# Kernel optimization log

Hardware: AMD Instinct MI355X
Metric: run time of the kernel (lower is better)

## Reference

```python
import jax, jax.numpy as jnp
import numpy as np

B, S, D, H = 16, 577, 1280, 16
HD = D // H  # 80
HALF = HD // 2  # 40


def setup_inputs() -> dict:
    key = jax.random.key(0)
    ks = jax.random.split(key, 8)
    hidden_states = jax.random.normal(ks[0], (B, S, D), dtype=jnp.float32)
    # 2D rotary frequencies: random angles -> unit-magnitude complex rotations
    angles = jax.random.uniform(ks[1], (S, HALF), dtype=jnp.float32) * (2.0 * np.pi)
    freqs_cos = jnp.cos(angles)
    freqs_sin = jnp.sin(angles)
    scale = 1.0 / np.sqrt(D)
    Wq = jax.random.normal(ks[2], (D, D), dtype=jnp.float32) * scale
    Wk = jax.random.normal(ks[3], (D, D), dtype=jnp.float32) * scale
    Wv = jax.random.normal(ks[4], (D, D), dtype=jnp.float32) * scale
    Wo = jax.random.normal(ks[5], (D, D), dtype=jnp.float32) * scale
    z = jnp.zeros((D,), dtype=jnp.float32)
    return {
        "hidden_states": hidden_states,
        "freqs_cos": freqs_cos,
        "freqs_sin": freqs_sin,
        "Wq": Wq, "bq": z, "Wk": Wk, "bk": z,
        "Wv": Wv, "bv": z, "Wo": Wo, "bo": z,
    }


def _apply_rotary(x, cos, sin):
    # x: [B,S,H,HD]; cos/sin: [S, HD/2]; interleaved complex pairs (even=real, odd=imag)
    xr = x[..., 0::2]
    xi = x[..., 1::2]
    c = cos[None, :, None, :]
    s = sin[None, :, None, :]
    out_r = xr * c - xi * s
    out_i = xr * s + xi * c
    # re-interleave pairs back to [..., HD]
    return jnp.stack([out_r, out_i], axis=-1).reshape(x.shape)


def reference(hidden_states, freqs_cos, freqs_sin, Wq, bq, Wk, bk, Wv, bv, Wo, bo):
    q = (hidden_states @ Wq.T + bq).reshape(B, S, H, HD)
    k = (hidden_states @ Wk.T + bk).reshape(B, S, H, HD)
    v = (hidden_states @ Wv.T + bv).reshape(B, S, H, HD)
    q = _apply_rotary(q, freqs_cos, freqs_sin)
    k = _apply_rotary(k, freqs_cos, freqs_sin)
    # [B,H,S,HD]
    q = q.transpose(0, 2, 1, 3)
    k = k.transpose(0, 2, 1, 3)
    v = v.transpose(0, 2, 1, 3)
    scale = 1.0 / np.sqrt(HD).astype(np.float32)
    scores = jnp.einsum("bhsd,bhtd->bhst", q, k) * scale
    probs = jax.nn.softmax(scores, axis=-1)
    attn = jnp.einsum("bhst,bhtd->bhsd", probs, v)
    attn = attn.transpose(0, 2, 1, 3).reshape(B, S, D)
    return attn @ Wo.T + bo
```

## Files before the change

### kernel.cpp

```cpp
#include <hip/hip_runtime.h>

#define B_N 16
#define S_N 577
#define D_N 1280
#define H_N 16
#define HD_N 80
#define HALF_N 40
#define M_N 9232
#define M_PAD 9344
#define M_PAD2 9472
#define K_N 1280
#define VT_S 608
#define QSCALE 0.11180339887498949f

typedef __bf16 bf16_t;
typedef bf16_t bf16x8 __attribute__((ext_vector_type(8)));
typedef float f32x4 __attribute__((ext_vector_type(4)));

__device__ __forceinline__ float bf2f(unsigned short u) {
    union { unsigned int i; float f; } x; x.i = ((unsigned int)u) << 16; return x.f;
}
__device__ __forceinline__ unsigned short f2bf(float f) {
    union { unsigned int i; float f; } x; x.f = f;
    unsigned int r = x.i + 0x7FFFu + ((x.i >> 16) & 1u);
    return (unsigned short)(r >> 16);
}

__device__ __forceinline__ void gld_lds16(const unsigned short* g, unsigned short* l) {
    __builtin_amdgcn_global_load_lds(
        (const __attribute__((address_space(1))) unsigned int*)g,
        (__attribute__((address_space(3))) unsigned int*)l,
        16, 0, 0);
}

__global__ __launch_bounds__(256) void cvt_kernel(const float* __restrict__ in,
                                                  unsigned short* __restrict__ out, int n4) {
    int i = blockIdx.x * 256 + threadIdx.x;
    if (i < n4) {
        float4 v = ((const float4*)in)[i];
        ushort4 o;
        o.x = f2bf(v.x); o.y = f2bf(v.y); o.z = f2bf(v.z); o.w = f2bf(v.w);
        ((ushort4*)out)[i] = o;
    }
}

#define W4_N (D_N * K_N / 4)
__global__ __launch_bounds__(256) void cvt4_kernel(
    const float* __restrict__ w0, const float* __restrict__ w1,
    const float* __restrict__ w2, const float* __restrict__ w3,
    unsigned short* __restrict__ out) {
    int i = blockIdx.x * 256 + threadIdx.x;
    if (i >= 4 * W4_N) return;
    int r = i / W4_N, j = i - r * W4_N;
    const float* src = (r == 0) ? w0 : (r == 1) ? w1 : (r == 2) ? w2 : w3;
    float4 v = ((const float4*)src)[j];
    ushort4 o;
    o.x = f2bf(v.x); o.y = f2bf(v.y); o.z = f2bf(v.z); o.w = f2bf(v.w);
    ((ushort4*)out)[i] = o;
}

#define PHASE_MFMA(AFR, BFR, MB) do {                                          \
    __builtin_amdgcn_s_setprio(1);                                             \
    _Pragma("unroll")                                                          \
    for (int mf_ = 0; mf_ < 4; ++mf_) {                                        \
        _Pragma("unroll")                                                      \
        for (int nf_ = 0; nf_ < 4; ++nf_)                                      \
            acc[(MB) + mf_][nf_] = __builtin_amdgcn_mfma_f32_16x16x32_bf16(    \
                (AFR)[mf_], (BFR)[nf_], acc[(MB) + mf_][nf_], 0, 0, 0);        \
    }                                                                          \
    __builtin_amdgcn_s_setprio(0);                                             \
} while (0)

#define BARRIER() do {                                                         \
    asm volatile("" ::: "memory");                                             \
    __builtin_amdgcn_s_barrier();                                              \
    __builtin_amdgcn_sched_barrier(0);                                         \
    asm volatile("" ::: "memory");                                             \
} while (0)

#define VMCNT8() do { asm volatile("s_waitcnt vmcnt(8)" ::: "memory"); } while (0)

#define KHALF(S, KK, ST_ODD, ST_EVEN) do {                                     \
    bf16x8 bfr[4], af[4];                                                      \
    _Pragma("unroll")                                                          \
    for (int f_ = 0; f_ < 4; ++f_) bfr[f_] = rdB(S, KK, f_);                   \
    _Pragma("unroll")                                                          \
    for (int f_ = 0; f_ < 4; ++f_) af[f_] = rdA(S, KK, f_);                    \
    ST_ODD;                                                                    \
    PHASE_MFMA(af, bfr, 0);                                                    \
    BARRIER();                                                                 \
    _Pragma("unroll")                                                          \
    for (int f_ = 0; f_ < 4; ++f_) af[f_] = rdA(S, KK, 4 + f_);                \
    ST_EVEN;                                                                   \
    PHASE_MFMA(af, bfr, 4);                                                    \
    VMCNT8();                                                                  \
    BARRIER();                                                                 \
} while (0)

__global__ __launch_bounds__(512, 2) void mgemm256_kernel(
    const unsigned short* __restrict__ A,
    const unsigned short* __restrict__ Wb,
    const float* __restrict__ b0, const float* __restrict__ b1,
    const float* __restrict__ b2,
    const float* __restrict__ cosb, const float* __restrict__ sinb,
    void* __restrict__ o0, void* __restrict__ o1, void* __restrict__ o2)
{
    extern __shared__ unsigned short smem[];
    unsigned short* const Asb = smem;
    unsigned short* const Bsb = smem + 4 * 8192;

    const int tid = threadIdx.x;
    const int wave = tid >> 6, lane = tid & 63;
    const int quad = lane >> 4, n = lane & 15;
    const int wm = wave >> 2, wn = wave & 3;
    const int m0 = blockIdx.y * 256, n0g = blockIdx.x * 256;

    const int srow = wave * 16 + (lane >> 2);
    const int scb  = (lane & 3) ^ ((lane >> 2) & 3);

    const unsigned short* gA = A  + (size_t)(m0  + srow) * K_N + scb * 8;
    const unsigned short* gB = Wb + (size_t)(n0g + srow) * K_N + scb * 8;

    f32x4 acc[8][4] = {};

    auto stA = [&](int s, int h, int kt) {
        unsigned short* l = Asb + (s * 2 + h) * 8192 + wave * 512;
        const unsigned short* g = gA + kt * 64 + h * 32;
        gld_lds16(g, l);
        gld_lds16(g + (size_t)128 * K_N, l + 4096);
    };
    auto stB = [&](int s, int h, int kt) {
        unsigned short* l = Bsb + (s * 2 + h) * 8192 + wave * 512;
        const unsigned short* g = gB + kt * 64 + h * 32;
        gld_lds16(g, l);
        gld_lds16(g + (size_t)128 * K_N, l + 4096);
    };

    const int sa_blk = (quad ^ (n & 3)) * 8;
    auto rdA = [&](int s, int kk, int mf) {
        return *(const bf16x8*)&Asb[(s * 2 + kk) * 8192 +
                                    (wm * 128 + mf * 16 + n) * 32 + sa_blk];
    };
    auto rdB = [&](int s, int kk, int nf) {
        return *(const bf16x8*)&Bsb[(s * 2 + kk) * 8192 +
                                    (wn * 64 + nf * 16 + n) * 32 + sa_blk];
    };

    stA(0, 0, 0); stB(0, 0, 0); stA(0, 1, 0); stB(0, 1, 0); stA(1, 0, 1); stB(1, 0, 1);
    VMCNT8();
    BARRIER();

    #pragma unroll 1
    for (int i = 0; i < 10; ++i) {
        const int tb  = 2 * i + 1;
        const int ta2 = (2 * i + 2 > 19) ? 19 : 2 * i + 2;
        const int tb2 = (2 * i + 3 > 19) ? 19 : 2 * i + 3;
        KHALF(0, 0, stA(1, 1, tb),  stB(1, 1, tb));
        KHALF(0, 1, stA(0, 0, ta2), stB(0, 0, ta2));
        KHALF(1, 0, stA(0, 1, ta2), stB(0, 1, ta2));
        KHALF(1, 1, stA(1, 0, tb2), stB(1, 0, tb2));
    }
    asm volatile("s_waitcnt vmcnt(0)" ::: "memory");

    const int wsel = blockIdx.x / 5;
    const float* bias = (wsel == 0) ? b0 : (wsel == 1) ? b1 : b2;
    unsigned short* out =
        (unsigned short*)((wsel == 0) ? o0 : (wsel == 1) ? o1 : o2);
    const int nloc0 = n0g - wsel * 1280 + wn * 64;
    const bool evn = (n & 1) == 0;

    #pragma unroll
    for (int mf = 0; mf < 8; ++mf) {
        #pragma unroll
        for (int r = 0; r < 4; ++r) {
            const int mrow = m0 + wm * 128 + mf * 16 + quad * 4 + r;
            const int b = mrow / S_N, s = mrow - b * S_N;
            const bool ok = mrow < M_N;
            #pragma unroll
            for (int nf = 0; nf < 4; ++nf) {
                const int ncol = nloc0 + nf * 16 + n;
                const int h = ncol / HD_N, hd = ncol - h * HD_N;
                float v = acc[mf][nf][r] + bias[ncol];
                if (wsel == 2) {
                    if (ok)
                        out[((size_t)(b * H_N + h) * HD_N + hd) * VT_S + s] = f2bf(v);
                } else {
                    float pv = __shfl_xor(v, 1);
                    float c  = cosb[s * HALF_N + (hd >> 1)];
                    float sn = sinb[s * HALF_N + (hd >> 1)];
                    float res = evn ? (v * c - pv * sn) : (pv * sn + v * c);
                    if (wsel == 0) res *= QSCALE;
                    if (ok)
                        out[((size_t)(b * H_N + h) * S_N + s) * HD_N + hd] = f2bf(res);
                }
            }
        }
    }
}

template <int MODE>
__global__ __launch_bounds__(256) void mgemm64_kernel(
    const unsigned short* __restrict__ A,
    const unsigned short* __restrict__ Wb,
    const float* __restrict__ b0,
    const float* __restrict__ cosb, const float* __restrict__ sinb,
    void* __restrict__ o0)
{
    __shared__ __align__(16) unsigned short As[2][128 * 64];
    __shared__ __align__(16) unsigned short Bs[2][128 * 64];

    const int tid = threadIdx.x;
    const int wave = tid >> 6, lane = tid & 63;
    const int quad = lane >> 4, n = lane & 15;
    const int wm = wave >> 1, wn = wave & 1;
    const int m0 = blockIdx.y * 128, n0g = blockIdx.x * 128;

    const int srow = lane >> 3;
    const int scol = (((lane & 7) ^ srow) * 8);

    const unsigned short* gA = A + (size_t)(m0 + wave * 32 + srow) * K_N + scol;
    const unsigned short* gB = Wb + (size_t)(n0g + wave * 32 + srow) * K_N + scol;
    const int lofs = wave * 32 * 64;

    f32x4 acc[4][4] = {};

    auto stage = [&](int pp, int k0) {
        unsigned short* lA = &As[pp][lofs];
        unsigned short* lB = &Bs[pp][lofs];
        #pragma unroll
        for (int i = 0; i < 4; ++i) {
            gld_lds16(gA + k0 + i * 8 * K_N, lA + i * 512);
            gld_lds16(gB + k0 + i * 8 * K_N, lB + i * 512);
        }
    };

    auto compute = [&](int pp) {
        #pragma unroll
        for (int kk = 0; kk < 2; ++kk) {
            const int sa = ((((kk << 2) | quad) ^ (n & 7)) * 8);
            bf16x8 af[4], bfr[4];
            #pragma unroll
            for (int mt = 0; mt < 4; ++mt)
                af[mt] = *(const bf16x8*)&As[pp][(wm * 64 + mt * 16 + n) * 64 + sa];
            #pragma unroll
            for (int nt = 0; nt < 4; ++nt)
                bfr[nt] = *(const bf16x8*)&Bs[pp][(wn * 64 + nt * 16 + n) * 64 + sa];
            #pragma unroll
            for (int mt = 0; mt < 4; ++mt)
                #pragma unroll
                for (int nt = 0; nt < 4; ++nt)
                    acc[mt][nt] = __builtin_amdgcn_mfma_f32_16x16x32_bf16(
                        af[mt], bfr[nt], acc[mt][nt], 0, 0, 0);
        }
    };

    stage(0, 0);

    #pragma unroll 2
    for (int t = 0; t < 19; ++t) {
        const int pp = t & 1;
        stage(pp ^ 1, (t + 1) * 64);
        asm volatile("s_waitcnt vmcnt(8)" ::: "memory");
        __builtin_amdgcn_s_barrier();
        compute(pp);
        __builtin_amdgcn_s_barrier();
    }
    asm volatile("s_waitcnt vmcnt(0)" ::: "memory");
    __builtin_amdgcn_s_barrier();
    compute(1);

    const int mbase = m0 + wm * 64;
    const int nbase = n0g + wn * 64;
    float* outp = (float*)o0;
    #pragma unroll
    for (int mt = 0; mt < 4; ++mt)
        #pragma unroll
        for (int nt = 0; nt < 4; ++nt) {
            const int ncol = nbase + nt * 16 + n;
            const float bv = b0[ncol];
            #pragma unroll
            for (int r = 0; r < 4; ++r) {
                int mrow = mbase + mt * 16 + quad * 4 + r;
                if (mrow < M_N)
                    outp[(size_t)mrow * D_N + ncol] = acc[mt][nt][r] + bv;
            }
        }
}

__global__ __launch_bounds__(256) void fattn_kernel(
    const unsigned short* __restrict__ qb,
    const unsigned short* __restrict__ kb,
    const unsigned short* __restrict__ vt,
    unsigned short* __restrict__ attn)
{
    __shared__ __align__(16) unsigned short Plds[4][2][2][16 * 32];

    const int tid = threadIdx.x;
    const int wave = tid >> 6, lane = tid & 63;
    const int quad = lane >> 4, n = lane & 15;

    const int bid = blockIdx.x;
    const int xcd = bid & 7, t = bid >> 3;
    const int qt = t % 5, hl = t / 5;
    const int bh = hl * 8 + xcd;
    const int q0 = qt * 128 + wave * 32;

    const bf16x8 zf{};
    const unsigned short* qrow0 = qb + ((size_t)bh * S_N + q0 + n) * HD_N;
    const unsigned short* qrow1 = qrow0 + 16 * HD_N;
    bf16x8 aq00 = *(const bf16x8*)(qrow0 + quad * 8);
    bf16x8 aq01 = *(const bf16x8*)(qrow0 + 32 + quad * 8);
    bf16x8 aq02 = (quad < 2) ? *(const bf16x8*)(qrow0 + 64 + quad * 8) : zf;
    bf16x8 aq10 = *(const bf16x8*)(qrow1 + quad * 8);
    bf16x8 aq11 = *(const bf16x8*)(qrow1 + 32 + quad * 8);
    bf16x8 aq12 = (quad < 2) ? *(const bf16x8*)(qrow1 + 64 + quad * 8) : zf;

    const bf16_t one = (bf16_t)1.0f;
    const bf16x8 vones_all = {one, one, one, one, one, one, one, one};
    const bf16x8 vones = (n == 0) ? vones_all : zf;

    f32x4 o0[6] = {};
    f32x4 o1[6] = {};

    const unsigned short* kbase = kb + (size_t)bh * S_N * HD_N;
    const unsigned short* vbase = vt + (size_t)bh * HD_N * VT_S;

    #pragma unroll 2
    for (int t0 = 0; t0 < 608; t0 += 32) {
        const int pp = (t0 >> 5) & 1;
        unsigned short* pl0 = &Plds[wave][pp][0][0];
        unsigned short* pl1 = &Plds[wave][pp][1][0];

        const unsigned short* krA = kbase + (size_t)(t0 + n) * HD_N;
        const unsigned short* krB = krA + 16 * HD_N;
        bf16x8 bA0 = *(const bf16x8*)(krA + quad * 8);
        bf16x8 bA1 = *(const bf16x8*)(krA + 32 + quad * 8);
        bf16x8 bA2 = (quad < 2) ? *(const bf16x8*)(krA + 64 + quad * 8) : zf;
        bf16x8 bB0 = *(const bf16x8*)(krB + quad * 8);
        bf16x8 bB1 = *(const bf16x8*)(krB + 32 + quad * 8);
        bf16x8 bB2 = (quad < 2) ? *(const bf16x8*)(krB + 64 + quad * 8) : zf;

        f32x4 c00{}, c01{}, c10{}, c11{};
        c00 = __builtin_amdgcn_mfma_f32_16x16x32_bf16(aq00, bA0, c00, 0, 0, 0);
        c00 = __builtin_amdgcn_mfma_f32_16x16x32_bf16(aq01, bA1, c00, 0, 0, 0);
        c00 = __builtin_amdgcn_mfma_f32_16x16x32_bf16(aq02, bA2, c00, 0, 0, 0);
        c01 = __builtin_amdgcn_mfma_f32_16x16x32_bf16(aq00, bB0, c01, 0, 0, 0);
        c01 = __builtin_amdgcn_mfma_f32_16x16x32_bf16(aq01, bB1, c01, 0, 0, 0);
        c01 = __builtin_amdgcn_mfma_f32_16x16x32_bf16(aq02, bB2, c01, 0, 0, 0);
        c10 = __builtin_amdgcn_mfma_f32_16x16x32_bf16(aq10, bA0, c10, 0, 0, 0);
        c10 = __builtin_amdgcn_mfma_f32_16x16x32_bf16(aq11, bA1, c10, 0, 0, 0);
        c10 = __builtin_amdgcn_mfma_f32_16x16x32_bf16(aq12, bA2, c10, 0, 0, 0);
        c11 = __builtin_amdgcn_mfma_f32_16x16x32_bf16(aq10, bB0, c11, 0, 0, 0);
        c11 = __builtin_amdgcn_mfma_f32_16x16x32_bf16(aq11, bB1, c11, 0, 0, 0);
        c11 = __builtin_amdgcn_mfma_f32_16x16x32_bf16(aq12, bB2, c11, 0, 0, 0);

        const bool mA = (t0 + n) >= S_N;
        const bool mB = (t0 + 16 + n) >= S_N;

        #pragma unroll
        for (int r = 0; r < 4; ++r) {
            float p00 = mA ? 0.0f : __expf(c00[r]);
            float p01 = mB ? 0.0f : __expf(c01[r]);
            float p10 = mA ? 0.0f : __expf(c10[r]);
            float p11 = mB ? 0.0f : __expf(c11[r]);
            pl0[(quad * 4 + r) * 32 + n]      = f2bf(p00);
            pl0[(quad * 4 + r) * 32 + 16 + n] = f2bf(p01);
            pl1[(quad * 4 + r) * 32 + n]      = f2bf(p10);
            pl1[(quad * 4 + r) * 32 + 16 + n] = f2bf(p11);
        }

        bf16x8 ap0 = *(const bf16x8*)(pl0 + n * 32 + quad * 8);
        bf16x8 ap1 = *(const bf16x8*)(pl1 + n * 32 + quad * 8);

        #pragma unroll
        for (int nt = 0; nt < 5; ++nt) {
            const unsigned short* vr = vbase + (size_t)(nt * 16 + n) * VT_S + t0 + quad * 8;
            bf16x8 bv = *(const bf16x8*)vr;
            o0[nt] = __builtin_amdgcn_mfma_f32_16x16x32_bf16(ap0, bv, o0[nt], 0, 0, 0);
            o1[nt] = __builtin_amdgcn_mfma_f32_16x16x32_bf16(ap1, bv, o1[nt], 0, 0, 0);
        }
        o0[5] = __builtin_amdgcn_mfma_f32_16x16x32_bf16(ap0, vones, o0[5], 0, 0, 0);
        o1[5] = __builtin_amdgcn_mfma_f32_16x16x32_bf16(ap1, vones, o1[5], 0, 0, 0);
    }

    const int b = bh >> 4, h = bh & 15;
    #pragma unroll
    for (int r = 0; r < 4; ++r) {
        float l0 = __shfl(o0[5][r], lane & 48);
        float l1 = __shfl(o1[5][r], lane & 48);
        float linv0 = 1.0f / l0, linv1 = 1.0f / l1;
        int s0 = q0 + quad * 4 + r;
        int s1 = s0 + 16;
        #pragma unroll
        for (int nt = 0; nt < 5; ++nt) {
            if (s0 < S_N)
                attn[((size_t)b * S_N + s0) * D_N + h * HD_N + nt * 16 + n] =
                    f2bf(o0[nt][r] * linv0);
            if (s1 < S_N)
                attn[((size_t)b * S_N + s1) * D_N + h * HD_N + nt * 16 + n] =
                    f2bf(o1[nt][r] * linv1);
        }
    }
}

extern "C" void kernel_launch(void* const* d_in, const int* in_sizes, int n_in,
                              void* d_out, int out_size, void* d_ws, size_t ws_size,
                              hipStream_t stream) {
    const float* hs = (const float*)d_in[0];
    const float* fc = (const float*)d_in[1];
    const float* fs = (const float*)d_in[2];
    const float* Wq = (const float*)d_in[3];
    const float* bq = (const float*)d_in[4];
    const float* Wk = (const float*)d_in[5];
    const float* bk = (const float*)d_in[6];
    const float* Wv = (const float*)d_in[7];
    const float* bv = (const float*)d_in[8];
    const float* Wo = (const float*)d_in[9];
    const float* bo = (const float*)d_in[10];
    float* out = (float*)d_out;

    char* ws = (char*)d_ws;
    size_t off = 0;
    auto alloc = [&](size_t bytes) {
        char* p = ws + off; off += (bytes + 255) & ~(size_t)255; return p;
    };
    unsigned short* hsb  = (unsigned short*)alloc((size_t)M_PAD2 * K_N * 2);
    unsigned short* qb   = (unsigned short*)alloc((size_t)M_N * K_N * 2 + 32768);
    unsigned short* kb   = (unsigned short*)alloc((size_t)M_N * K_N * 2 + 32768);
    unsigned short* vt   = (unsigned short*)alloc((size_t)B_N * H_N * HD_N * VT_S * 2);
    unsigned short* Wall = (unsigned short*)alloc((size_t)4 * D_N * K_N * 2);

    const int HS4 = M_N * K_N / 4;
    dim3 blk(256);

    cvt_kernel<<<(HS4 + 255) / 256, blk, 0, stream>>>(hs, hsb, HS4);
    cvt4_kernel<<<(4 * W4_N + 255) / 256, blk, 0, stream>>>(Wq, Wk, Wv, Wo, Wall);

    (void)hipFuncSetAttribute(reinterpret_cast<const void*>(&mgemm256_kernel),
                              hipFuncAttributeMaxDynamicSharedMemorySize, 131072);
    mgemm256_kernel<<<dim3(15, 37), dim3(512), 131072, stream>>>(
        hsb, Wall, bq, bk, bv, fc, fs, qb, kb, vt);

    fattn_kernel<<<dim3(1280), blk, 0, stream>>>(qb, kb, vt, hsb );

    mgemm64_kernel<3><<<dim3(10, 73), blk, 0, stream>>>(
        hsb, Wall + 3 * (size_t)D_N * K_N, bo, fc, fs, out);
}
```

Baseline: 467.6 us.

## Simplify QKV GEMM to double-buffered K=32 stages with smaller LDS footprint

Replaces the four-stage, 64-wide K pipeline in the fused QKV GEMM, which used 128 KB of dynamic LDS, with a simple two-stage double buffer of 32-wide K slices in 64 KB of static LDS. The swizzle changes to match the new layout, and launch bounds ask for 4 blocks per CU instead of 2. The goal is more resident workgroups to hide latency instead of deep software prefetch. In exchange there are two barriers per 32-wide K step instead of per half-tile, a shallower prefetch distance, and register pressure under the tighter launch bound that may cause spills.

```diff
diff --git a/kernel.cpp b/kernel.cpp
--- a/kernel.cpp
+++ b/kernel.cpp
@@ -78,26 +78,7 @@
     asm volatile("" ::: "memory");                                             \
 } while (0)
 
-#define VMCNT8() do { asm volatile("s_waitcnt vmcnt(8)" ::: "memory"); } while (0)
-
-#define KHALF(S, KK, ST_ODD, ST_EVEN) do {                                     \
-    bf16x8 bfr[4], af[4];                                                      \
-    _Pragma("unroll")                                                          \
-    for (int f_ = 0; f_ < 4; ++f_) bfr[f_] = rdB(S, KK, f_);                   \
-    _Pragma("unroll")                                                          \
-    for (int f_ = 0; f_ < 4; ++f_) af[f_] = rdA(S, KK, f_);                    \
-    ST_ODD;                                                                    \
-    PHASE_MFMA(af, bfr, 0);                                                    \
-    BARRIER();                                                                 \
-    _Pragma("unroll")                                                          \
-    for (int f_ = 0; f_ < 4; ++f_) af[f_] = rdA(S, KK, 4 + f_);                \
-    ST_EVEN;                                                                   \
-    PHASE_MFMA(af, bfr, 4);                                                    \
-    VMCNT8();                                                                  \
-    BARRIER();                                                                 \
-} while (0)
-
-__global__ __launch_bounds__(512, 2) void mgemm256_kernel(
+__global__ __launch_bounds__(512, 4) void mgemm256_kernel(
     const unsigned short* __restrict__ A,
     const unsigned short* __restrict__ Wb,
     const float* __restrict__ b0, const float* __restrict__ b1,
@@ -105,9 +86,8 @@
     const float* __restrict__ cosb, const float* __restrict__ sinb,
     void* __restrict__ o0, void* __restrict__ o1, void* __restrict__ o2)
 {
-    extern __shared__ unsigned short smem[];
-    unsigned short* const Asb = smem;
-    unsigned short* const Bsb = smem + 4 * 8192;
+    __shared__ __align__(16) unsigned short Asb[2][8192];
+    __shared__ __align__(16) unsigned short Bsb[2][8192];
 
     const int tid = threadIdx.x;
     const int wave = tid >> 6, lane = tid & 63;
@@ -116,49 +96,51 @@
     const int m0 = blockIdx.y * 256, n0g = blockIdx.x * 256;
 
     const int srow = wave * 16 + (lane >> 2);
-    const int scb  = (lane & 3) ^ ((lane >> 2) & 3);
+    const int scb  = (lane & 3) ^ ((lane >> 3) & 3);
 
     const unsigned short* gA = A  + (size_t)(m0  + srow) * K_N + scb * 8;
     const unsigned short* gB = Wb + (size_t)(n0g + srow) * K_N + scb * 8;
 
     f32x4 acc[8][4] = {};
 
-    auto stA = [&](int s, int h, int kt) {
-        unsigned short* l = Asb + (s * 2 + h) * 8192 + wave * 512;
-        const unsigned short* g = gA + kt * 64 + h * 32;
-        gld_lds16(g, l);
-        gld_lds16(g + (size_t)128 * K_N, l + 4096);
-    };
-    auto stB = [&](int s, int h, int kt) {
-        unsigned short* l = Bsb + (s * 2 + h) * 8192 + wave * 512;
-        const unsigned short* g = gB + kt * 64 + h * 32;
-        gld_lds16(g, l);
-        gld_lds16(g + (size_t)128 * K_N, l + 4096);
-    };
-
-    const int sa_blk = (quad ^ (n & 3)) * 8;
-    auto rdA = [&](int s, int kk, int mf) {
-        return *(const bf16x8*)&Asb[(s * 2 + kk) * 8192 +
-                                    (wm * 128 + mf * 16 + n) * 32 + sa_blk];
-    };
-    auto rdB = [&](int s, int kk, int nf) {
-        return *(const bf16x8*)&Bsb[(s * 2 + kk) * 8192 +
-                                    (wn * 64 + nf * 16 + n) * 32 + sa_blk];
-    };
-
-    stA(0, 0, 0); stB(0, 0, 0); stA(0, 1, 0); stB(0, 1, 0); stA(1, 0, 1); stB(1, 0, 1);
-    VMCNT8();
-    BARRIER();
-
-    #pragma unroll 1
-    for (int i = 0; i < 10; ++i) {
-        const int tb  = 2 * i + 1;
-        const int ta2 = (2 * i + 2 > 19) ? 19 : 2 * i + 2;
-        const int tb2 = (2 * i + 3 > 19) ? 19 : 2 * i + 3;
-        KHALF(0, 0, stA(1, 1, tb),  stB(1, 1, tb));
-        KHALF(0, 1, stA(0, 0, ta2), stB(0, 0, ta2));
-        KHALF(1, 0, stA(0, 1, ta2), stB(0, 1, ta2));
-        KHALF(1, 1, stA(1, 0, tb2), stB(1, 0, tb2));
+    auto stage = [&](int s, int kt) {
+        unsigned short* lA = &Asb[s][wave * 512];
+        unsigned short* lB = &Bsb[s][wave * 512];
+        const unsigned short* a = gA + kt * 32;
+        const unsigned short* b = gB + kt * 32;
+        gld_lds16(a, lA);
+        gld_lds16(a + (size_t)128 * K_N, lA + 4096);
+        gld_lds16(b, lB);
+        gld_lds16(b + (size_t)128 * K_N, lB + 4096);
+    };
+
+    const int sa_blk = (quad ^ ((n >> 1) & 3)) * 8;
+    auto rdA = [&](int s, int mf) {
+        return *(const bf16x8*)&Asb[s][(wm * 128 + mf * 16 + n) * 32 + sa_blk];
+    };
+    auto rdB = [&](int s, int nf) {
+        return *(const bf16x8*)&Bsb[s][(wn * 64 + nf * 16 + n) * 32 + sa_blk];
+    };
+
+    stage(0, 0);
+
+    #pragma unroll 2
+    for (int t = 0; t < 40; ++t) {
+        const int s = t & 1;
+        const int tn = (t + 1 < 40) ? t + 1 : 39;
+        stage(s ^ 1, tn);
+        asm volatile("s_waitcnt vmcnt(4)" ::: "memory");
+        BARRIER();
+        bf16x8 bfr[4], af[4];
+        #pragma unroll
+        for (int f = 0; f < 4; ++f) bfr[f] = rdB(s, f);
+        #pragma unroll
+        for (int f = 0; f < 4; ++f) af[f] = rdA(s, f);
+        PHASE_MFMA(af, bfr, 0);
+        #pragma unroll
+        for (int f = 0; f < 4; ++f) af[f] = rdA(s, 4 + f);
+        PHASE_MFMA(af, bfr, 4);
+        BARRIER();
     }
     asm volatile("s_waitcnt vmcnt(0)" ::: "memory");
 
@@ -436,9 +418,7 @@
     cvt_kernel<<<(HS4 + 255) / 256, blk, 0, stream>>>(hs, hsb, HS4);
     cvt4_kernel<<<(4 * W4_N + 255) / 256, blk, 0, stream>>>(Wq, Wk, Wv, Wo, Wall);
 
-    (void)hipFuncSetAttribute(reinterpret_cast<const void*>(&mgemm256_kernel),
-                              hipFuncAttributeMaxDynamicSharedMemorySize, 131072);
-    mgemm256_kernel<<<dim3(15, 37), dim3(512), 131072, stream>>>(
+    mgemm256_kernel<<<dim3(15, 37), dim3(512), 0, stream>>>(
         hsb, Wall, bq, bk, bv, fc, fs, qb, kb, vt);
 
     fattn_kernel<<<dim3(1280), blk, 0, stream>>>(qb, kb, vt, hsb );
```

New measurement: 1.344 ms. +187.5%, slower.
